# Kernel tuning notes

Measured on AMD Instinct MI355X. Metric: run time of the kernel, lower is better.

Reference implementation:

```python
import jax, jax.numpy as jnp
import numpy as np

PASS = 8        # pass_through_size
FLOW = 16       # flow_size
TRANS = FLOW - PASS  # transform_size = 8
NBINS = 64
HID = 1024


def _conditioner(yA, w1, b1, w2, b2, w3, b3):
    # MLP producing unnormalized positive bin widths Q: [B, TRANS, NBINS]
    h = jax.nn.relu(yA @ w1 + b1)
    h = jax.nn.relu(h @ w2 + b2)
    q = jax.nn.softplus(h @ w3 + b3) + 1e-6  # positivity for slopes
    return q.reshape(-1, TRANS, NBINS)


def setup_inputs() -> dict:
    key = jax.random.key(0)
    ks = jax.random.split(key, 4)
    B = 65536
    y = jax.random.uniform(ks[0], (B, FLOW + 1), dtype=jnp.float32)
    w1 = jax.random.normal(ks[1], (PASS, HID), dtype=jnp.float32) / np.sqrt(PASS)
    w2 = jax.random.normal(ks[2], (HID, HID), dtype=jnp.float32) / np.sqrt(HID)
    w3 = jax.random.normal(ks[3], (HID, TRANS * NBINS), dtype=jnp.float32) / np.sqrt(HID)
    return {
        "y": y,
        "w1": w1, "b1": jnp.zeros((HID,), jnp.float32),
        "w2": w2, "b2": jnp.zeros((HID,), jnp.float32),
        "w3": w3, "b3": jnp.zeros((TRANS * NBINS,), jnp.float32),
    }


def reference(y, w1, b1, w2, b2, w3, b3):
    yA = y[:, :PASS]                      # [B, PASS]
    yB = y[:, PASS:FLOW]                  # [B, TRANS]
    jac = y[:, FLOW:FLOW + 1]             # [B, 1]

    Q = _conditioner(yA, w1, b1, w2, b2, w3, b3)  # [B, TRANS, NBINS]
    Qsum = jnp.cumsum(Q, axis=-1)
    Qnorms = Qsum[:, :, -1:]
    Q = Q / (Qnorms / NBINS)              # slopes per bin
    Qsum = Qsum / Qnorms                  # normalized CDF knots (last == 1)

    # searchsorted(side='left') per row: count of knots strictly below value
    ybins = jnp.sum(Qsum < yB[..., None], axis=-1)          # [B, TRANS] int32
    ybins = jnp.clip(ybins, 0, NBINS - 1)                   # guard fp edge case

    paddedQsum = jnp.pad(Qsum, ((0, 0), (0, 0), (1, 0)))    # prepend 0 knot
    offsets = jnp.take_along_axis(paddedQsum, ybins[..., None], axis=-1)[..., 0]
    slopes = jnp.take_along_axis(Q, ybins[..., None], axis=-1)[..., 0]

    xB = (yB - offsets) / slopes + ybins.astype(jnp.float32) / NBINS
    jac = jac * jnp.prod(1.0 / slopes, axis=-1, keepdims=True)
    return jnp.concatenate((yA, xB, jac), axis=-1)          # [B, FLOW+1]
```

## Files before the change

### kernel.cpp

```cpp
#include <hip/hip_runtime.h>
#include <hip/hip_fp16.h>

#define HID 1024
#define QCOLS 512
#define KP 2048
#define NT 48

typedef _Float16 f16x8 __attribute__((ext_vector_type(8)));
typedef float f32x4 __attribute__((ext_vector_type(4)));

__global__ void tconv_both(const float* __restrict__ w2, __half* __restrict__ w2t,
                           const float* __restrict__ w3, __half* __restrict__ w3t) {
  __shared__ float tile[32][33];
  const int z = blockIdx.z;
  const int N = z ? QCOLS : HID;
  if (blockIdx.x * 32 >= N) return;
  const float* src = z ? w3 : w2;
  __half* dst = z ? w3t : w2t;
  int n0 = blockIdx.x * 32, k0 = blockIdx.y * 32;
  int tx = threadIdx.x, ty = threadIdx.y;
  for (int i = ty; i < 32; i += 8)
    tile[i][tx] = src[(size_t)(k0 + i) * N + n0 + tx];
  __syncthreads();
  for (int i = ty; i < 32; i += 8) {
    float v = tile[tx][i] * 256.f;
    __half h = __float2half(v);
    size_t o = (size_t)(n0 + i) * KP + k0 + tx;
    dst[o] = h;
    dst[o + 1024] = __float2half(v - __half2float(h));
  }
}

__global__ __launch_bounds__(256)
void h1k(const float* __restrict__ y, const float* __restrict__ w1,
         const float* __restrict__ b1, __half* __restrict__ h1,
         int row0, int nrows) {
  const int t = threadIdx.x & 127;
  const int rl = threadIdx.x >> 7;
  const long r = (long)blockIdx.x * 2 + rl;
  if (r >= nrows) return;
  const float* yr = y + (size_t)(row0 + r) * 17;
  float yv[8];
#pragma unroll
  for (int k = 0; k < 8; ++k) yv[k] = yr[k];
  const int c0 = t * 8;
  f32x4 a0 = *(const f32x4*)(b1 + c0);
  f32x4 a1 = *(const f32x4*)(b1 + c0 + 4);
#pragma unroll
  for (int k = 0; k < 8; ++k) {
    const f32x4 w0 = *(const f32x4*)(w1 + k * HID + c0);
    const f32x4 w1v = *(const f32x4*)(w1 + k * HID + c0 + 4);
#pragma unroll
    for (int j = 0; j < 4; ++j) {
      a0[j] = fmaf(yv[k], w0[j], a0[j]);
      a1[j] = fmaf(yv[k], w1v[j], a1[j]);
    }
  }
  f16x8 hi, lo;
#pragma unroll
  for (int j = 0; j < 8; ++j) {
    float v = fmaxf(j < 4 ? a0[j] : a1[j - 4], 0.f) * 64.f;
    _Float16 h = (_Float16)v;
    hi[j] = h;
    lo[j] = (_Float16)(v - (float)h);
  }
  *(f16x8*)(h1 + (size_t)r * KP + c0) = hi;
  *(f16x8*)(h1 + (size_t)r * KP + c0 + 1024) = lo;
}

template <int ACT, int BM, int BN>
__device__ __forceinline__
void gemm1b_body(const __half* __restrict__ A, const __half* __restrict__ Bt,
                 const float* __restrict__ bias, __half* __restrict__ Co,
                 float* __restrict__ Cf, int ldc) {
  constexpr int MFRAG = BM / 32;
  constexpr int NFRAG = BN / 64;
  constexpr int SLOT = (BM + BN) * 64;
  constexpr int LA = BM / 128;
  constexpr int LB = BN / 128;
  constexpr int LPS = LA + LB;
  __shared__ char lds[3 * SLOT];
  const int tid = threadIdx.x;
  const int lane = tid & 63, wave = tid >> 6;
  const int p = lane & 15, ql = lane >> 4;
  const int wm = wave >> 2, wn = wave & 3;

  const int gx = gridDim.x, nwg = gx * gridDim.y;
  const int bid = blockIdx.y * gx + blockIdx.x;
  const int q8 = nwg >> 3, r8 = nwg & 7;
  const int xcd = bid & 7, lxi = bid >> 3;
  const int swz = (xcd < r8 ? xcd * (q8 + 1) : r8 * (q8 + 1) + (xcd - r8) * q8) + lxi;
  const size_t row_blk = (size_t)(swz / gx) * BM;
  const size_t col_blk = (size_t)(swz % gx) * BN;

  int a_off[MFRAG], b_off[NFRAG];
#pragma unroll
  for (int m = 0; m < MFRAG; ++m) {
    int r = wm * (BM / 2) + m * 16 + p;
    a_off[m] = r * 64 + ((ql ^ ((r >> 1) & 3)) << 4);
  }
#pragma unroll
  for (int n = 0; n < NFRAG; ++n) {
    int r = wn * (BN / 4) + n * 16 + p;
    b_off[n] = r * 64 + ((ql ^ ((r >> 1) & 3)) << 4);
  }

  auto gload = [&](const __half* g, char* l) {
    __builtin_amdgcn_global_load_lds((__attribute__((address_space(1))) void*)g,
        (__attribute__((address_space(3))) void*)l, 16, 0, 0);
  };

  auto stage = [&](int q, int slot) {
    int kt = q >> 1; if (kt > NT - 1) kt = NT - 1;
    const int h = q & 1;
    const int lk = kt * 64;
    const int ak = ((lk >= 2048) ? 1024 : 0) + (lk & 1023) + h * 32;
    const int bk = ((lk >= 1024 && lk < 2048) ? 1024 : 0) + (lk & 1023) + h * 32;
    char* pa = lds + slot * SLOT;
    char* pb = pa + BM * 64;
#pragma unroll
    for (int i = 0; i < LA; ++i) {
      const int idx = tid + i * 512;
      const int sr = idx >> 2, sq = (idx & 3) ^ ((sr >> 1) & 3);
      gload(A + (row_blk + sr) * (size_t)KP + ak + sq * 8, pa + idx * 16);
    }
#pragma unroll
    for (int i = 0; i < LB; ++i) {
      const int idx = tid + i * 512;
      const int sr = idx >> 2, sq = (idx & 3) ^ ((sr >> 1) & 3);
      gload(Bt + (col_blk + sr) * (size_t)KP + bk + sq * 8, pb + idx * 16);
    }
  };

  stage(0, 0);
  stage(1, 1);

  f32x4 acc[MFRAG][NFRAG] = {};

  int cur = 0;
  for (int ph = 0; ph < NT * 2; ++ph) {
    if constexpr (LPS == 4) asm volatile("s_waitcnt vmcnt(4)" ::: "memory");
    else                    asm volatile("s_waitcnt vmcnt(3)" ::: "memory");
    __builtin_amdgcn_sched_barrier(0);
    __builtin_amdgcn_s_barrier();
    __builtin_amdgcn_sched_barrier(0);

    const char* base = lds + cur * SLOT;
    const char* pB = base + BM * 64;
    f16x8 af[MFRAG], bfr[NFRAG];
#pragma unroll
    for (int m = 0; m < MFRAG; ++m) af[m] = *(const f16x8*)(base + a_off[m]);
#pragma unroll
    for (int n = 0; n < NFRAG; ++n) bfr[n] = *(const f16x8*)(pB + b_off[n]);

    const int nslot = cur == 0 ? 2 : cur - 1;
    stage(ph + 2, nslot);
    __builtin_amdgcn_sched_barrier(0);

    __builtin_amdgcn_s_setprio(1);
#pragma unroll
    for (int m = 0; m < MFRAG; ++m)
#pragma unroll
      for (int n = 0; n < NFRAG; ++n)
        acc[m][n] = __builtin_amdgcn_mfma_f32_16x16x32_f16(af[m], bfr[n], acc[m][n], 0, 0, 0);
    __builtin_amdgcn_s_setprio(0);
    cur = cur == 2 ? 0 : cur + 1;
  }

  const float unscale = 1.f / 16384.f;
#pragma unroll
  for (int n = 0; n < NFRAG; ++n) {
    const size_t col = col_blk + wn * (BN / 4) + n * 16 + p;
    const float bv = bias[col];
#pragma unroll
    for (int m = 0; m < MFRAG; ++m) {
      const size_t row0 = row_blk + wm * (BM / 2) + m * 16 + ql * 4;
#pragma unroll
      for (int j = 0; j < 4; ++j) {
        float v = acc[m][n][j] * unscale + bv;
        const size_t o = (row0 + j) * (size_t)ldc + col;
        if constexpr (ACT == 0) {
          float r = fmaxf(v, 0.f) * 64.f;
          __half hh = __float2half(r);
          Co[o] = hh;
          Co[o + 1024] = __float2half(r - __half2float(hh));
        } else {
          float sp = fmaxf(v, 0.f) + log1pf(expf(-fabsf(v)));
          Cf[o] = sp + 1e-6f;
        }
      }
    }
  }
}

__global__ __launch_bounds__(512, 2)
void g2relu(const __half* __restrict__ A, const __half* __restrict__ B,
            const float* __restrict__ bias, __half* __restrict__ Co) {
  gemm1b_body<0, 256, 256>(A, B, bias, Co, nullptr, KP);
}

__global__ __launch_bounds__(512, 4)
void g3soft(const __half* __restrict__ A, const __half* __restrict__ B,
            const float* __restrict__ bias, float* __restrict__ Cf) {
  gemm1b_body<1, 128, 256>(A, B, bias, nullptr, Cf, QCOLS);
}

__global__ __launch_bounds__(256)
void pwl_epi(const float* __restrict__ y, const float* __restrict__ q,
             float* __restrict__ out, int row0, int nrows) {
  const int wave = threadIdx.x >> 6, lane = threadIdx.x & 63;
  const int r = blockIdx.x * 4 + wave;
  if (r >= nrows) return;
  const float* yr = y + (size_t)(row0 + r) * 17;
  float* orow = out + (size_t)(row0 + r) * 17;
  const float* qr = q + (size_t)r * QCOLS;
  float prod_inv = 1.f;
#pragma unroll
  for (int t = 0; t < 8; ++t) {
    const float qv = qr[t * 64 + lane];
    float s = qv;
#pragma unroll
    for (int d = 1; d < 64; d <<= 1) {
      float u = __shfl_up(s, d);
      if (lane >= d) s += u;
    }
    const float total = __shfl(s, 63);
    const float sn = s / total;
    const float dnorm = total * 0.015625f;
    const float slope_l = qv / dnorm;
    const float yb = yr[8 + t];
    const unsigned long long m = __ballot(sn < yb);
    int bin = (int)__popcll(m);
    bin = bin > 63 ? 63 : bin;
    const float off_g = __shfl(sn, bin > 0 ? bin - 1 : 0);
    const float off = (bin == 0) ? 0.f : off_g;
    const float sl = __shfl(slope_l, bin);
    const float xB = (yb - off) / sl + (float)bin * 0.015625f;
    if (lane == t) orow[8 + t] = xB;
    prod_inv *= (1.f / sl);
  }
  if (lane < 8) orow[lane] = yr[lane];
  if (lane == 8) orow[16] = yr[16] * prod_inv;
}

extern "C" void kernel_launch(void* const* d_in, const int* in_sizes, int n_in,
                              void* d_out, int out_size, void* d_ws, size_t ws_size,
                              hipStream_t stream) {
  const float* y  = (const float*)d_in[0];
  const float* w1 = (const float*)d_in[1];
  const float* b1 = (const float*)d_in[2];
  const float* w2 = (const float*)d_in[3];
  const float* b2 = (const float*)d_in[4];
  const float* w3 = (const float*)d_in[5];
  const float* b3 = (const float*)d_in[6];
  float* out = (float*)d_out;
  const long Btot = in_sizes[0] / 17;

  char* ws = (char*)d_ws;
  __half* w2t = (__half*)ws;
  __half* w3t = (__half*)(ws + (4u << 20));
  const size_t fixed = (size_t)6 << 20;

  const size_t avail = ws_size > fixed ? ws_size - fixed : 0;
  long maxrows = (long)(avail / 8192);
  long chunk = 256;
  for (long c = 65536; c >= 256; c >>= 1) {
    if (c <= maxrows && c <= Btot) { chunk = c; break; }
  }

  __half* h1buf = (__half*)(ws + fixed);
  __half* h2buf = (__half*)(ws + fixed + (size_t)chunk * 4096);
  float* qbuf = (float*)h1buf;

  tconv_both<<<dim3(32, 32, 2), dim3(32, 8), 0, stream>>>(w2, w2t, w3, w3t);

  for (long row0 = 0; row0 < Btot; row0 += chunk) {
    const int nr = (int)((Btot - row0 < chunk) ? (Btot - row0) : chunk);
    h1k<<<(nr + 1) / 2, 256, 0, stream>>>(y, w1, b1, h1buf, (int)row0, nr);
    g2relu<<<dim3(HID / 256, nr / 256), 512, 0, stream>>>(h1buf, w2t, b2, h2buf);
    g3soft<<<dim3(QCOLS / 256, nr / 128), 512, 0, stream>>>(h2buf, w3t, b3, qbuf);
    pwl_epi<<<(nr + 3) / 4, 256, 0, stream>>>(y, qbuf, out, (int)row0, nr);
  }
}
```

Baseline: 890.1 us.

## Replace triple-buffered LDS pipeline with double buffer and register prefetch

Both GEMM kernels move from a three-slot LDS ring with one barrier per K-step to a two-slot LDS buffer. The next step's fragments are prefetched into a second register set while the current MFMAs run, with the loop unrolled by two. This halves LDS use and drops the slot-rotation arithmetic. In exchange it adds full vmcnt(0)/lgkmcnt(0) waits before each barrier, which may expose global-load latency, and it lowers g3soft's launch-bounds occupancy hint from 4 to 2.

```diff
diff --git a/kernel.cpp b/kernel.cpp
--- a/kernel.cpp
+++ b/kernel.cpp
@@ -70,16 +70,15 @@
 
 template <int ACT, int BM, int BN>
 __device__ __forceinline__
-void gemm1b_body(const __half* __restrict__ A, const __half* __restrict__ Bt,
-                 const float* __restrict__ bias, __half* __restrict__ Co,
-                 float* __restrict__ Cf, int ldc) {
+void gemm_rdb_body(const __half* __restrict__ A, const __half* __restrict__ Bt,
+                   const float* __restrict__ bias, __half* __restrict__ Co,
+                   float* __restrict__ Cf, int ldc) {
   constexpr int MFRAG = BM / 32;
   constexpr int NFRAG = BN / 64;
   constexpr int SLOT = (BM + BN) * 64;
   constexpr int LA = BM / 128;
   constexpr int LB = BN / 128;
-  constexpr int LPS = LA + LB;
-  __shared__ char lds[3 * SLOT];
+  __shared__ char lds[2 * SLOT];
   const int tid = threadIdx.x;
   const int lane = tid & 63, wave = tid >> 6;
   const int p = lane & 15, ql = lane >> 4;
@@ -132,39 +131,66 @@
     }
   };
 
+  f16x8 afA[MFRAG], bfA[NFRAG], afB[MFRAG], bfB[NFRAG];
+  f32x4 acc[MFRAG][NFRAG] = {};
+
   stage(0, 0);
   stage(1, 1);
-
-  f32x4 acc[MFRAG][NFRAG] = {};
-
-  int cur = 0;
-  for (int ph = 0; ph < NT * 2; ++ph) {
-    if constexpr (LPS == 4) asm volatile("s_waitcnt vmcnt(4)" ::: "memory");
-    else                    asm volatile("s_waitcnt vmcnt(3)" ::: "memory");
+  asm volatile("s_waitcnt vmcnt(%0)" :: "n"(LA + LB) : "memory");
+  __builtin_amdgcn_s_barrier();
+  {
+    const char* b0 = lds;
+    const char* p0 = lds + BM * 64;
+#pragma unroll
+    for (int m = 0; m < MFRAG; ++m) afA[m] = *(const f16x8*)(b0 + a_off[m]);
+#pragma unroll
+    for (int n = 0; n < NFRAG; ++n) bfA[n] = *(const f16x8*)(p0 + b_off[n]);
+  }
+
+  for (int ph = 0; ph < NT * 2; ph += 2) {
+    asm volatile("s_waitcnt lgkmcnt(0)" ::: "memory");
+    asm volatile("s_waitcnt vmcnt(0)" ::: "memory");
     __builtin_amdgcn_sched_barrier(0);
     __builtin_amdgcn_s_barrier();
     __builtin_amdgcn_sched_barrier(0);
-
-    const char* base = lds + cur * SLOT;
-    const char* pB = base + BM * 64;
-    f16x8 af[MFRAG], bfr[NFRAG];
-#pragma unroll
-    for (int m = 0; m < MFRAG; ++m) af[m] = *(const f16x8*)(base + a_off[m]);
-#pragma unroll
-    for (int n = 0; n < NFRAG; ++n) bfr[n] = *(const f16x8*)(pB + b_off[n]);
-
-    const int nslot = cur == 0 ? 2 : cur - 1;
-    stage(ph + 2, nslot);
+    {
+      const char* b1 = lds + SLOT;
+      const char* p1 = b1 + BM * 64;
+#pragma unroll
+      for (int m = 0; m < MFRAG; ++m) afB[m] = *(const f16x8*)(b1 + a_off[m]);
+#pragma unroll
+      for (int n = 0; n < NFRAG; ++n) bfB[n] = *(const f16x8*)(p1 + b_off[n]);
+      stage(ph + 2, 0);
+    }
+    __builtin_amdgcn_s_setprio(1);
+#pragma unroll
+    for (int m = 0; m < MFRAG; ++m)
+#pragma unroll
+      for (int n = 0; n < NFRAG; ++n)
+        acc[m][n] = __builtin_amdgcn_mfma_f32_16x16x32_f16(afA[m], bfA[n], acc[m][n], 0, 0, 0);
+    __builtin_amdgcn_s_setprio(0);
+
+    asm volatile("s_waitcnt lgkmcnt(0)" ::: "memory");
+    asm volatile("s_waitcnt vmcnt(0)" ::: "memory");
     __builtin_amdgcn_sched_barrier(0);
-
+    __builtin_amdgcn_s_barrier();
+    __builtin_amdgcn_sched_barrier(0);
+    {
+      const char* b0 = lds;
+      const char* p0 = lds + BM * 64;
+#pragma unroll
+      for (int m = 0; m < MFRAG; ++m) afA[m] = *(const f16x8*)(b0 + a_off[m]);
+#pragma unroll
+      for (int n = 0; n < NFRAG; ++n) bfA[n] = *(const f16x8*)(p0 + b_off[n]);
+      stage(ph + 3, 1);
+    }
     __builtin_amdgcn_s_setprio(1);
 #pragma unroll
     for (int m = 0; m < MFRAG; ++m)
 #pragma unroll
       for (int n = 0; n < NFRAG; ++n)
-        acc[m][n] = __builtin_amdgcn_mfma_f32_16x16x32_f16(af[m], bfr[n], acc[m][n], 0, 0, 0);
+        acc[m][n] = __builtin_amdgcn_mfma_f32_16x16x32_f16(afB[m], bfB[n], acc[m][n], 0, 0, 0);
     __builtin_amdgcn_s_setprio(0);
-    cur = cur == 2 ? 0 : cur + 1;
   }
 
   const float unscale = 1.f / 16384.f;
@@ -196,13 +222,13 @@
 __global__ __launch_bounds__(512, 2)
 void g2relu(const __half* __restrict__ A, const __half* __restrict__ B,
             const float* __restrict__ bias, __half* __restrict__ Co) {
-  gemm1b_body<0, 256, 256>(A, B, bias, Co, nullptr, KP);
-}
-
-__global__ __launch_bounds__(512, 4)
+  gemm_rdb_body<0, 256, 256>(A, B, bias, Co, nullptr, KP);
+}
+
+__global__ __launch_bounds__(512, 2)
 void g3soft(const __half* __restrict__ A, const __half* __restrict__ B,
             const float* __restrict__ bias, float* __restrict__ Cf) {
-  gemm1b_body<1, 128, 256>(A, B, bias, nullptr, Cf, QCOLS);
+  gemm_rdb_body<1, 128, 256>(A, B, bias, nullptr, Cf, QCOLS);
 }
 
 __global__ __launch_bounds__(256)
```

Result: slower. 938.6 us (+5.5%).
